# Optimization experiments

Hardware: AMD Instinct MI355X
Metric: run time of the kernel (lower is better)

## Reference

```python
import jax, jax.numpy as jnp
import numpy as np

N_NODES = 50000
N_EDGES = 1000000
HIDDEN = 64
NUM_GRAPHS = 512
EPS = 1e-5


def _instance_norm(x, seg, num_graphs):
    # per-graph, per-channel normalization (PyG InstanceNorm, affine=False)
    ones = jnp.ones((x.shape[0], 1), x.dtype)
    cnt = jnp.clip(jax.ops.segment_sum(ones, seg, num_segments=num_graphs), 1.0)
    mean = jax.ops.segment_sum(x, seg, num_segments=num_graphs) / cnt
    xc = x - mean[seg]
    var = jax.ops.segment_sum(xc * xc, seg, num_segments=num_graphs) / cnt
    return xc * jax.lax.rsqrt(var + EPS)[seg]


def setup_inputs() -> dict:
    key = jax.random.key(0)
    ks = jax.random.split(key, 10)
    emb = jax.random.normal(ks[0], (N_NODES, HIDDEN), jnp.float32)
    edge_index = jax.random.randint(ks[1], (2, N_EDGES), 0, N_NODES, jnp.int64 if jax.config.read('jax_enable_x64') else jnp.int32)
    batch = jnp.sort(jax.random.randint(ks[2], (N_NODES,), 0, NUM_GRAPHS))
    h = HIDDEN
    # channels = [2h, 4h, h, 1]
    W1 = jax.random.normal(ks[3], (2 * h, 4 * h), jnp.float32) * 0.05
    b1 = jnp.zeros((4 * h,), jnp.float32)
    W2 = jax.random.normal(ks[4], (4 * h, h), jnp.float32) * 0.05
    b2 = jnp.zeros((h,), jnp.float32)
    W3 = jax.random.normal(ks[5], (h, 1), jnp.float32) * 0.05
    b3 = jnp.zeros((1,), jnp.float32)
    return {"emb": emb, "W1": W1, "b1": b1, "W2": W2, "b2": b2,
            "W3": W3, "b3": b3, "edge_index": edge_index, "batch": batch}


def reference(emb, W1, b1, W2, b2, W3, b3, edge_index, batch):
    col, row = edge_index[0], edge_index[1]
    f12 = jnp.concatenate([emb[col], emb[row]], axis=-1)  # [E, 2h]
    seg = batch[col]  # per-edge graph id
    x = f12 @ W1 + b1                                      # [E, 4h]
    x = jax.nn.relu(_instance_norm(x, seg, NUM_GRAPHS))
    x = x @ W2 + b2                                        # [E, h]
    x = jax.nn.relu(_instance_norm(x, seg, NUM_GRAPHS))
    return x @ W3 + b3                                     # [E, 1]
```

## Files before the change

kernel.cpp:

```cpp
#include <hip/hip_runtime.h>
#include <hip/hip_bf16.h>

#define EDGES 1000000
#define NNODES 50000
#define NG 512
#define NTILES 15625
#define NCOLB 50176

typedef __attribute__((ext_vector_type(8))) short bf16x8;
typedef __attribute__((ext_vector_type(4))) float f32x4;

__device__ __forceinline__ unsigned short f2bf(float f){
  unsigned u = __float_as_uint(f);
  u += 0x7fffu + ((u >> 16) & 1u);
  return (unsigned short)(u >> 16);
}
__device__ __forceinline__ float bf2f(unsigned short h){
  return __uint_as_float(((unsigned)h) << 16);
}
__device__ __forceinline__ unsigned pk2bf(float x, float y){
  __hip_bfloat162 h = __float22bfloat162_rn(make_float2(x, y));
  union { __hip_bfloat162 h; unsigned u; } cv; cv.h = h;
  return cv.u;
}
__device__ __forceinline__ void gload_lds16(const void* g, void* l){
  __builtin_amdgcn_global_load_lds(
      (const __attribute__((address_space(1))) unsigned int*)g,
      (__attribute__((address_space(3))) unsigned int*)l, 16, 0, 0);
}
__device__ __forceinline__ int xcd_swizzle(int bid, int nb){
  int nb8 = nb & ~7;
  if (bid >= nb8) return bid;
  int per = nb8 >> 3;
  return (bid & 7) * per + (bid >> 3);
}

__global__ void prep_all(const float* __restrict__ emb, const float* __restrict__ W1,
                         const float* __restrict__ W2,
                         unsigned short* __restrict__ emb_bf,
                         unsigned short* __restrict__ w1tn, unsigned short* __restrict__ w2t){
  int i = blockIdx.x * 256 + threadIdx.x;
  if (i < NNODES * 64){
    emb_bf[i] = f2bf(emb[i]);
  } else {
    int j = i - NNODES * 64;
    if (j < 32768){
      int jj = j >> 6, k = j & 63;
      float v = (jj < 256) ? W1[k * 256 + jj] : W1[(k + 64) * 256 + (jj - 256)];
      w1tn[j] = f2bf(v);
    } else {
      int jj = j - 32768;
      if (jj < 16384){
        int n = jj >> 8, p = jj & 255;
        int korig = (p & ~127) | ((p & 7) << 4) | ((p >> 3) & 15);
        w2t[jj] = f2bf(W2[korig * 64 + n]);
      }
    }
  }
}

__global__ void hists(const int* __restrict__ ei, const int* __restrict__ batch,
                      unsigned* __restrict__ hist, unsigned* __restrict__ chist){
  __shared__ unsigned h[NG];
  int t = threadIdx.x;
  h[t] = 0; h[t + 256] = 0;
  __syncthreads();
  for (int i = 0; i < 4; i++){
    int e = blockIdx.x * 1024 + i * 256 + t;
    if (e < EDGES){
      int cn = ei[e];
      atomicAdd(&chist[cn], 1u);
      atomicAdd(&h[batch[cn]], 1u);
    }
  }
  __syncthreads();
  atomicAdd(&hist[t], h[t]);
  atomicAdd(&hist[t + 256], h[t + 256]);
}

__global__ void col_scan1(const unsigned* __restrict__ chist, unsigned* __restrict__ cpre,
                          unsigned* __restrict__ bsum){
  __shared__ unsigned s[256];
  int t = threadIdx.x;
  int i = blockIdx.x * 256 + t;
  unsigned v = (i < NNODES) ? chist[i] : 0u;
  s[t] = v;
  __syncthreads();
  for (int o = 1; o < 256; o <<= 1){
    unsigned u = (t >= o) ? s[t - o] : 0u;
    __syncthreads();
    s[t] += u;
    __syncthreads();
  }
  cpre[i] = s[t] - v;
  if (t == 255) bsum[blockIdx.x] = s[255];
}

__global__ void col_scan2(unsigned* __restrict__ bsum){
  __shared__ unsigned s[256];
  int t = threadIdx.x;
  unsigned v = (t < 196) ? bsum[t] : 0u;
  s[t] = v;
  __syncthreads();
  for (int o = 1; o < 256; o <<= 1){
    unsigned u = (t >= o) ? s[t - o] : 0u;
    __syncthreads();
    s[t] += u;
    __syncthreads();
  }
  if (t < 196) bsum[t] = s[t] - v;
}

__global__ void col_scan3(unsigned* __restrict__ cpre, const unsigned* __restrict__ bsum){
  int i = blockIdx.x * 256 + threadIdx.x;
  cpre[i] += bsum[blockIdx.x];
}

__global__ void col_scatter(const int* __restrict__ ei, const int* __restrict__ batch,
                            unsigned* __restrict__ cpre, int4* __restrict__ emeta){
  for (int i = 0; i < 4; i++){
    int e = blockIdx.x * 1024 + i * 256 + threadIdx.x;
    if (e < EDGES){
      int cn = ei[e];
      int pos = (int)atomicAdd(&cpre[cn], 1u);
      emeta[pos] = make_int4(cn, ei[EDGES + e], batch[cn], e);
    }
  }
}

__global__ __launch_bounds__(256) void node_gemm(
    const unsigned short* __restrict__ emb_bf, const unsigned short* __restrict__ w1tn,
    unsigned short* __restrict__ P)
{
  __shared__ unsigned short As[64 * 72];
  int t = threadIdx.x;
  int n0 = blockIdx.x * 64;
  {
    int nl = t >> 2, part = t & 3;
    int node = n0 + nl; if (node >= NNODES) node = 0;
    const int4* src = (const int4*)(emb_bf + node * 64 + part * 16);
    int4* dst = (int4*)(As + nl * 72 + part * 16);
    dst[0] = src[0]; dst[1] = src[1];
  }
  __syncthreads();
  int w = t >> 6, lane = t & 63, q = lane >> 4, c = lane & 15;
  f32x4 acc[4][8];
  for (int a = 0; a < 4; a++) for (int b = 0; b < 8; b++) for (int r = 0; r < 4; r++) acc[a][b][r] = 0.f;
  for (int k0 = 0; k0 < 64; k0 += 32){
    bf16x8 af[4];
    for (int tt = 0; tt < 4; tt++) af[tt] = *(const bf16x8*)(As + (tt * 16 + c) * 72 + k0 + q * 8);
    for (int n4 = 0; n4 < 8; n4++){
      bf16x8 bw = *(const bf16x8*)(w1tn + (w * 128 + n4 * 16 + c) * 64 + k0 + q * 8);
      for (int tt = 0; tt < 4; tt++)
        acc[tt][n4] = __builtin_amdgcn_mfma_f32_16x16x32_bf16(af[tt], bw, acc[tt][n4], 0, 0, 0);
    }
  }
  for (int tt = 0; tt < 4; tt++){
    for (int r = 0; r < 4; r++){
      int node = n0 + tt * 16 + q * 4 + r;
      if (node < NNODES){
        uint4 pk;
        pk.x = pk2bf(acc[tt][0][r], acc[tt][1][r]);
        pk.y = pk2bf(acc[tt][2][r], acc[tt][3][r]);
        pk.z = pk2bf(acc[tt][4][r], acc[tt][5][r]);
        pk.w = pk2bf(acc[tt][6][r], acc[tt][7][r]);
        *(uint4*)(P + (size_t)node * 512 + w * 128 + c * 8) = pk;
      }
    }
  }
}

__global__ __launch_bounds__(256, 5) void k1_gather(
    const unsigned short* __restrict__ P, const int4* __restrict__ emeta,
    float* __restrict__ sum1, float* __restrict__ sqs1)
{
  __shared__ float ls[1024];
  int t = threadIdx.x;
  int bid = xcd_swizzle(blockIdx.x, gridDim.x);
  int tile0 = bid * 8;
  for (int i = t; i < 1024; i += 256) ls[i] = 0.f;
  int s0 = emeta[tile0 * 64].z;
  int elast = tile0 * 64 + 511; if (elast >= EDGES) elast = EDGES - 1;
  int s1 = emeta[elast].z;
  __syncthreads();

  int w = t >> 6, lane = t & 63, c4 = lane * 4;

  float sm0 = 0.f, sm1 = 0.f, sm2 = 0.f, sm3 = 0.f;
  float q0 = 0.f, q1 = 0.f, q2 = 0.f, q3 = 0.f;
  int curs = -1;

  auto FLUSH = [&](int s){
    if (s == s0 || s == s1){
      float* base = ls + ((s == s0) ? 0 : 512) + c4;
      atomicAdd(base + 0, sm0); atomicAdd(base + 1, sm1);
      atomicAdd(base + 2, sm2); atomicAdd(base + 3, sm3);
      atomicAdd(base + 256, q0); atomicAdd(base + 257, q1);
      atomicAdd(base + 258, q2); atomicAdd(base + 259, q3);
    } else {
      float* sp = sum1 + s * 256 + c4;
      float* qp = sqs1 + s * 256 + c4;
      atomicAdd(sp + 0, sm0); atomicAdd(sp + 1, sm1); atomicAdd(sp + 2, sm2); atomicAdd(sp + 3, sm3);
      atomicAdd(qp + 0, q0);  atomicAdd(qp + 1, q1);  atomicAdd(qp + 2, q2);  atomicAdd(qp + 3, q3);
    }
    sm0 = sm1 = sm2 = sm3 = 0.f; q0 = q1 = q2 = q3 = 0.f;
  };

  for (int ti = 0; ti < 2; ti++){
    int tile = tile0 + w * 2 + ti;
    if (tile >= NTILES) continue;
    int4 me = emeta[tile * 64 + lane];
    int sseg = __builtin_amdgcn_readlane(me.z, 0);
    bool uni = (__ballot(me.z == sseg) == ~0ull);
    if (uni){
      if (sseg != curs){
        if (curs >= 0) FLUSH(curs);
        curs = sseg;
      }
      ushort4 rv[3][4], cv[3][4];
      #pragma unroll
      for (int g = 0; g < 2; g++){
        #pragma unroll
        for (int j = 0; j < 4; j++){
          int e = g * 4 + j;
          int re = __builtin_amdgcn_readlane(me.y, e);
          int ce = __builtin_amdgcn_readlane(me.x, e);
          rv[g][j] = *(const ushort4*)(P + (size_t)re * 512 + 256 + c4);
          cv[g][j] = *(const ushort4*)(P + (size_t)ce * 512 + c4);
        }
      }
      #pragma unroll
      for (int g = 0; g < 16; g++){
        if (g < 14){
          int bn = (g + 2) % 3;
          #pragma unroll
          for (int j = 0; j < 4; j++){
            int e = (g + 2) * 4 + j;
            int re = __builtin_amdgcn_readlane(me.y, e);
            int ce = __builtin_amdgcn_readlane(me.x, e);
            rv[bn][j] = *(const ushort4*)(P + (size_t)re * 512 + 256 + c4);
            cv[bn][j] = *(const ushort4*)(P + (size_t)ce * 512 + c4);
          }
        }
        int b = g % 3;
        #pragma unroll
        for (int j = 0; j < 4; j++){
          float x0 = bf2f(cv[b][j].x) + bf2f(rv[b][j].x);
          float x1 = bf2f(cv[b][j].y) + bf2f(rv[b][j].y);
          float x2v = bf2f(cv[b][j].z) + bf2f(rv[b][j].z);
          float x3 = bf2f(cv[b][j].w) + bf2f(rv[b][j].w);
          sm0 += x0; q0 += x0 * x0;
          sm1 += x1; q1 += x1 * x1;
          sm2 += x2v; q2 += x2v * x2v;
          sm3 += x3; q3 += x3 * x3;
        }
      }
    } else {
      int cprev = -1;
      ushort4 a = make_ushort4(0, 0, 0, 0);
      for (int e = 0; e < 64; e++){
        int ce = __builtin_amdgcn_readlane(me.x, e);
        int re = __builtin_amdgcn_readlane(me.y, e);
        int s = __builtin_amdgcn_readlane(me.z, e);
        if (s != curs){
          if (curs >= 0) FLUSH(curs);
          curs = s;
        }
        if (ce != cprev){ a = *(const ushort4*)(P + (size_t)ce * 512 + c4); cprev = ce; }
        ushort4 b = *(const ushort4*)(P + (size_t)re * 512 + 256 + c4);
        float x0 = bf2f(a.x) + bf2f(b.x);
        float x1 = bf2f(a.y) + bf2f(b.y);
        float x2v = bf2f(a.z) + bf2f(b.z);
        float x3 = bf2f(a.w) + bf2f(b.w);
        sm0 += x0; q0 += x0 * x0;
        sm1 += x1; q1 += x1 * x1;
        sm2 += x2v; q2 += x2v * x2v;
        sm3 += x3; q3 += x3 * x3;
      }
    }
  }
  if (curs >= 0) FLUSH(curs);

  __syncthreads();
  atomicAdd(&sum1[s0 * 256 + t], ls[t]);
  atomicAdd(&sqs1[s0 * 256 + t], ls[256 + t]);
  if (s1 != s0){
    atomicAdd(&sum1[s1 * 256 + t], ls[512 + t]);
    atomicAdd(&sqs1[s1 * 256 + t], ls[768 + t]);
  }
}

__global__ void finalize1(const float* __restrict__ sum1, const float* __restrict__ sqs1,
                          const unsigned* __restrict__ hist, float* __restrict__ r1,
                          float* __restrict__ mr1){
  int i = blockIdx.x * 256 + threadIdx.x;
  int g = i >> 8;
  float cnt = fmaxf((float)hist[g], 1.f);
  float m = sum1[i] / cnt;
  float v = sqs1[i] / cnt - m * m;
  v = fmaxf(v, 0.f);
  float r = rsqrtf(v + 1e-5f);
  r1[i] = r;
  mr1[i] = m * r;
}

__global__ void finalize2(const float* __restrict__ sum2, const float* __restrict__ sqs2,
                          const unsigned* __restrict__ hist, float* __restrict__ r2,
                          float* __restrict__ mr2){
  int i = blockIdx.x * 256 + threadIdx.x;
  int g = i >> 6;
  float cnt = fmaxf((float)hist[g], 1.f);
  float m = sum2[i] / cnt;
  float v = sqs2[i] / cnt - m * m;
  v = fmaxf(v, 0.f);
  float r = rsqrtf(v + 1e-5f);
  r2[i] = r;
  mr2[i] = m * r;
}

__global__ __launch_bounds__(256, 4) void k2_fused(
    const unsigned short* __restrict__ P, const unsigned short* __restrict__ w2t,
    const int4* __restrict__ emeta,
    const float* __restrict__ r1, const float* __restrict__ mr1,
    float* __restrict__ sum2, float* __restrict__ sqs2,
    unsigned short* __restrict__ x2t)
{
  __shared__ unsigned short Y[64 * 256];
  __shared__ int segl[64];
  __shared__ short rsegA[64];
  __shared__ unsigned char rloA[65];
  __shared__ int nrunS;
  int t = threadIdx.x;
  int bid = xcd_swizzle(blockIdx.x, gridDim.x);
  int p0 = bid * 64;
  int w = t >> 6, lane = t & 63, q = lane >> 4, c = lane & 15;
  int c4 = lane * 4;
  int elb0 = w * 16;
  int4 me = emeta[p0 + elb0 + (lane & 15)];

  #pragma unroll
  for (int pp = 0; pp < 8; pp++){
    int r0 = __builtin_amdgcn_readlane(me.y, 2 * pp);
    int r1n = __builtin_amdgcn_readlane(me.y, 2 * pp + 1);
    int node = (lane < 32) ? r0 : r1n;
    const unsigned short* g = P + (size_t)node * 512 + 256 + (lane & 31) * 8;
    gload_lds16(g, &Y[(elb0 + 2 * pp) * 256]);
  }

  int cprev = __builtin_amdgcn_readlane(me.x, 0);
  ushort4 a = *(const ushort4*)(P + (size_t)cprev * 512 + c4);
  int s0g = __builtin_amdgcn_readlane(me.z, 0);
  float4 r4  = *(const float4*)(r1  + s0g * 256 + c4);
  float4 mr4 = *(const float4*)(mr1 + s0g * 256 + c4);

  if (t < 64) segl[t] = emeta[p0 + t].z;
  if (w == 0){
    int sN = segl[lane];
    int nxt = (lane < 63) ? segl[lane + 1] : sN;
    unsigned long long mask = __ballot(sN != nxt);
    if (lane == 0){
      if (mask == 0ull){
        nrunS = 1; rloA[0] = 0; rloA[1] = 64; rsegA[0] = (short)sN;
      } else {
        int n = 0, cur = segl[0];
        rsegA[0] = (short)cur; rloA[0] = 0;
        for (int i = 1; i < 64; i++)
          if (segl[i] != cur){ cur = segl[i]; n++; rsegA[n] = (short)cur; rloA[n] = (unsigned char)i; }
        rloA[n + 1] = 64; nrunS = n + 1;
      }
    }
  }
  __syncthreads();
  int nrun = nrunS;
  bool uni = (nrun == 1);

  ushort4 bb[16];
  #pragma unroll
  for (int e = 0; e < 16; e++)
    bb[e] = *(const ushort4*)(Y + (elb0 + e) * 256 + c4);

  #pragma unroll
  for (int e = 0; e < 16; e++){
    int ce = __builtin_amdgcn_readlane(me.x, e);
    if (ce != cprev){ a = *(const ushort4*)(P + (size_t)ce * 512 + c4); cprev = ce; }
    float4 rr4 = r4, mm4 = mr4;
    if (!uni){
      int s = __builtin_amdgcn_readlane(me.z, e);
      rr4 = *(const float4*)(r1  + s * 256 + c4);
      mm4 = *(const float4*)(mr1 + s * 256 + c4);
    }
    float y0 = fmaxf(0.f, (bf2f(a.x) + bf2f(bb[e].x)) * rr4.x - mm4.x);
    float y1 = fmaxf(0.f, (bf2f(a.y) + bf2f(bb[e].y)) * rr4.y - mm4.y);
    float y2 = fmaxf(0.f, (bf2f(a.z) + bf2f(bb[e].z)) * rr4.z - mm4.z);
    float y3 = fmaxf(0.f, (bf2f(a.w) + bf2f(bb[e].w)) * rr4.w - mm4.w);
    uint2 pk;
    pk.x = pk2bf(y0, y1);
    pk.y = pk2bf(y2, y3);
    int row = elb0 + e;
    *(uint2*)((char*)Y + row * 512 + ((lane * 8) ^ ((row & 7) << 4))) = pk;
  }
  __syncthreads();

  f32x4 acc2[4];
  for (int tt = 0; tt < 4; tt++) for (int r = 0; r < 4; r++) acc2[tt][r] = 0.f;
  int ch2 = w * 16 + c;
  int swzr = (c & 7) << 4;
  for (int kc = 0; kc < 8; kc++){
    bf16x8 bfr = *(const bf16x8*)(w2t + ch2 * 256 + kc * 32 + q * 8);
    int kb = (kc * 64 + q * 16) ^ swzr;
    for (int tt = 0; tt < 4; tt++){
      bf16x8 afr = *(const bf16x8*)((const char*)Y + (tt * 16 + c) * 512 + kb);
      acc2[tt] = __builtin_amdgcn_mfma_f32_16x16x32_bf16(afr, bfr, acc2[tt], 0, 0, 0);
    }
  }

  if (uni){
    int s = segl[0];
    float sm = 0.f, sq = 0.f;
    for (int tt = 0; tt < 4; tt++)
      for (int r = 0; r < 4; r++){
        float v = acc2[tt][r];
        sm += v; sq += v * v;
      }
    sm += __shfl_xor(sm, 16); sq += __shfl_xor(sq, 16);
    sm += __shfl_xor(sm, 32); sq += __shfl_xor(sq, 32);
    if (q == 0){
      atomicAdd(&sum2[s * 64 + ch2], sm);
      atomicAdd(&sqs2[s * 64 + ch2], sq);
    }
  } else {
    for (int rr = 0; rr < nrun; rr++){
      int s = rsegA[rr], lo = rloA[rr], hi = rloA[rr + 1];
      float sm = 0.f, sq = 0.f;
      for (int tt = 0; tt < 4; tt++){
        int elb = tt * 16 + q * 4;
        for (int r = 0; r < 4; r++){
          int el = elb + r;
          if (el >= lo && el < hi){
            float v = acc2[tt][r];
            sm += v; sq += v * v;
          }
        }
      }
      sm += __shfl_xor(sm, 16); sq += __shfl_xor(sq, 16);
      sm += __shfl_xor(sm, 32); sq += __shfl_xor(sq, 32);
      if (q == 0){
        atomicAdd(&sum2[s * 64 + ch2], sm);
        atomicAdd(&sqs2[s * 64 + ch2], sq);
      }
    }
  }
  for (int tt = 0; tt < 4; tt++){
    uint2 pk;
    pk.x = pk2bf(acc2[tt][0], acc2[tt][1]);
    pk.y = pk2bf(acc2[tt][2], acc2[tt][3]);
    *(uint2*)(x2t + (size_t)ch2 * EDGES + p0 + tt * 16 + q * 4) = pk;
  }
}

__global__ __launch_bounds__(256) void k3_out(
    const unsigned short* __restrict__ x2t, const int4* __restrict__ emeta,
    const float* __restrict__ r2, const float* __restrict__ mr2,
    const float* __restrict__ W3, const float* __restrict__ b3, float* __restrict__ out)
{
  int pp4 = (blockIdx.x * 256 + threadIdx.x) * 4;
  if (pp4 >= EDGES) return;
  int4 m0 = emeta[pp4 + 0];
  int4 m1 = emeta[pp4 + 1];
  int4 m2 = emeta[pp4 + 2];
  int4 m3 = emeta[pp4 + 3];
  float a0 = 0.f, a1 = 0.f, a2 = 0.f, a3 = 0.f;
  if (m0.z == m3.z && m0.z == m1.z && m0.z == m2.z){
    const float* rp = r2  + m0.z * 64;
    const float* mp = mr2 + m0.z * 64;
    #pragma unroll 8
    for (int ch = 0; ch < 64; ch++){
      ushort4 v = *(const ushort4*)(x2t + (size_t)ch * EDGES + pp4);
      float rr = rp[ch], mm = mp[ch], wv = W3[ch];
      a0 += fmaxf(0.f, bf2f(v.x) * rr - mm) * wv;
      a1 += fmaxf(0.f, bf2f(v.y) * rr - mm) * wv;
      a2 += fmaxf(0.f, bf2f(v.z) * rr - mm) * wv;
      a3 += fmaxf(0.f, bf2f(v.w) * rr - mm) * wv;
    }
  } else {
    #pragma unroll 8
    for (int ch = 0; ch < 64; ch++){
      ushort4 v = *(const ushort4*)(x2t + (size_t)ch * EDGES + pp4);
      float wv = W3[ch];
      a0 += fmaxf(0.f, bf2f(v.x) * r2[m0.z * 64 + ch] - mr2[m0.z * 64 + ch]) * wv;
      a1 += fmaxf(0.f, bf2f(v.y) * r2[m1.z * 64 + ch] - mr2[m1.z * 64 + ch]) * wv;
      a2 += fmaxf(0.f, bf2f(v.z) * r2[m2.z * 64 + ch] - mr2[m2.z * 64 + ch]) * wv;
      a3 += fmaxf(0.f, bf2f(v.w) * r2[m3.z * 64 + ch] - mr2[m3.z * 64 + ch]) * wv;
    }
  }
  float bv = b3[0];
  out[m0.w] = a0 + bv;
  out[m1.w] = a1 + bv;
  out[m2.w] = a2 + bv;
  out[m3.w] = a3 + bv;
}

extern "C" void kernel_launch(void* const* d_in, const int* in_sizes, int n_in,
                              void* d_out, int out_size, void* d_ws, size_t ws_size,
                              hipStream_t stream)
{
  (void)in_sizes; (void)n_in; (void)out_size;
  const float* emb = (const float*)d_in[0];
  const float* W1  = (const float*)d_in[1];
  const float* W2  = (const float*)d_in[3];
  const float* W3  = (const float*)d_in[5];
  const float* b3  = (const float*)d_in[6];
  const int* ei    = (const int*)d_in[7];
  const int* batch = (const int*)d_in[8];
  float* out = (float*)d_out;

  char* p = (char*)d_ws;
  size_t off = 0;
  auto take = [&](size_t n) -> char* {
    char* r = p + off;
    off += (n + 255) & ~(size_t)255;
    return r;
  };

  unsigned short* emb_bf = (unsigned short*)take((size_t)NNODES * 64 * 2);
  unsigned short* w1tn   = (unsigned short*)take(32768 * 2);
  unsigned short* w2t    = (unsigned short*)take(16384 * 2);
  int4* emeta = (int4*)take((size_t)EDGES * 16);
  unsigned short* P   = (unsigned short*)take((size_t)NNODES * 512 * 2);
  unsigned short* x2t = (unsigned short*)take((size_t)EDGES * 64 * 2);
  float* r1  = (float*)take(512 * 256 * 4);
  float* mr1 = (float*)take(512 * 256 * 4);
  float* r2  = (float*)take(512 * 64 * 4);
  float* mr2 = (float*)take(512 * 64 * 4);
  unsigned* cpre = (unsigned*)take(NCOLB * 4);
  unsigned* bsum = (unsigned*)take(256 * 4);
  char* zbase = p + off;
  unsigned* hist  = (unsigned*)take(NG * 4);
  unsigned* chist = (unsigned*)take(NCOLB * 4);
  float* sum1 = (float*)take(512 * 256 * 4);
  float* sqs1 = (float*)take(512 * 256 * 4);
  float* sum2 = (float*)take(512 * 64 * 4);
  float* sqs2 = (float*)take(512 * 64 * 4);
  size_t zsize = (size_t)((p + off) - zbase);

  if (ws_size < off) return;

  hipMemsetAsync(zbase, 0, zsize, stream);
  prep_all<<<12692, 256, 0, stream>>>(emb, W1, W2, emb_bf, w1tn, w2t);
  hists<<<977, 256, 0, stream>>>(ei, batch, hist, chist);
  col_scan1<<<196, 256, 0, stream>>>(chist, cpre, bsum);
  col_scan2<<<1, 256, 0, stream>>>(bsum);
  col_scan3<<<196, 256, 0, stream>>>(cpre, bsum);
  col_scatter<<<977, 256, 0, stream>>>(ei, batch, cpre, emeta);
  node_gemm<<<(NNODES + 63) / 64, 256, 0, stream>>>(emb_bf, w1tn, P);
  k1_gather<<<(NTILES + 7) / 8, 256, 0, stream>>>(P, emeta, sum1, sqs1);
  finalize1<<<512, 256, 0, stream>>>(sum1, sqs1, hist, r1, mr1);
  k2_fused<<<NTILES, 256, 0, stream>>>(P, w2t, emeta, r1, mr1, sum2, sqs2, x2t);
  finalize2<<<128, 256, 0, stream>>>(sum2, sqs2, hist, r2, mr2);
  k3_out<<<977, 256, 0, stream>>>(x2t, emeta, r2, mr2, W3, b3, out);
}
```

Measured before the change: 495.5 us.

## Merge preprocessing kernels into fewer launches and use nontemporal x2t traffic

Fuses the histogram and bf16 conversion kernels into one launch by splitting blocks by role. It also merges the column scatter with the node GEMM, folding the block-offset scan add into the scatter so the col_scan3 launch goes away. Separately, the x2t intermediate is written and read with nontemporal hints to reduce cache pollution. This cuts three kernel launches and their serialization gaps, at the cost of heterogeneous blocks inside one grid.

```diff
diff --git a/kernel.cpp b/kernel.cpp
--- a/kernel.cpp
+++ b/kernel.cpp
@@ -6,6 +6,8 @@
 #define NG 512
 #define NTILES 15625
 #define NCOLB 50176
+#define HBLK 977
+#define GBLK 782
 
 typedef __attribute__((ext_vector_type(8))) short bf16x8;
 typedef __attribute__((ext_vector_type(4))) float f32x4;
@@ -35,47 +37,48 @@
   return (bid & 7) * per + (bid >> 3);
 }
 
-__global__ void prep_all(const float* __restrict__ emb, const float* __restrict__ W1,
-                         const float* __restrict__ W2,
-                         unsigned short* __restrict__ emb_bf,
-                         unsigned short* __restrict__ w1tn, unsigned short* __restrict__ w2t){
-  int i = blockIdx.x * 256 + threadIdx.x;
-  if (i < NNODES * 64){
-    emb_bf[i] = f2bf(emb[i]);
-  } else {
-    int j = i - NNODES * 64;
-    if (j < 32768){
-      int jj = j >> 6, k = j & 63;
-      float v = (jj < 256) ? W1[k * 256 + jj] : W1[(k + 64) * 256 + (jj - 256)];
-      w1tn[j] = f2bf(v);
-    } else {
-      int jj = j - 32768;
-      if (jj < 16384){
-        int n = jj >> 8, p = jj & 255;
-        int korig = (p & ~127) | ((p & 7) << 4) | ((p >> 3) & 15);
-        w2t[jj] = f2bf(W2[korig * 64 + n]);
-      }
-    }
-  }
-}
-
-__global__ void hists(const int* __restrict__ ei, const int* __restrict__ batch,
-                      unsigned* __restrict__ hist, unsigned* __restrict__ chist){
+__global__ void prep_hists(const float* __restrict__ emb, const float* __restrict__ W1,
+                           const float* __restrict__ W2,
+                           const int* __restrict__ ei, const int* __restrict__ batch,
+                           unsigned short* __restrict__ emb_bf,
+                           unsigned short* __restrict__ w1tn, unsigned short* __restrict__ w2t,
+                           unsigned* __restrict__ hist, unsigned* __restrict__ chist){
   __shared__ unsigned h[NG];
   int t = threadIdx.x;
-  h[t] = 0; h[t + 256] = 0;
-  __syncthreads();
-  for (int i = 0; i < 4; i++){
-    int e = blockIdx.x * 1024 + i * 256 + t;
-    if (e < EDGES){
-      int cn = ei[e];
-      atomicAdd(&chist[cn], 1u);
-      atomicAdd(&h[batch[cn]], 1u);
-    }
-  }
-  __syncthreads();
-  atomicAdd(&hist[t], h[t]);
-  atomicAdd(&hist[t + 256], h[t + 256]);
+  if (blockIdx.x < HBLK){
+    h[t] = 0; h[t + 256] = 0;
+    __syncthreads();
+    for (int i = 0; i < 4; i++){
+      int e = blockIdx.x * 1024 + i * 256 + t;
+      if (e < EDGES){
+        int cn = ei[e];
+        atomicAdd(&chist[cn], 1u);
+        atomicAdd(&h[batch[cn]], 1u);
+      }
+    }
+    __syncthreads();
+    atomicAdd(&hist[t], h[t]);
+    atomicAdd(&hist[t + 256], h[t + 256]);
+  } else {
+    int i = (blockIdx.x - HBLK) * 256 + t;
+    if (i < NNODES * 64){
+      emb_bf[i] = f2bf(emb[i]);
+    } else {
+      int j = i - NNODES * 64;
+      if (j < 32768){
+        int jj = j >> 6, k = j & 63;
+        float v = (jj < 256) ? W1[k * 256 + jj] : W1[(k + 64) * 256 + (jj - 256)];
+        w1tn[j] = f2bf(v);
+      } else {
+        int jj = j - 32768;
+        if (jj < 16384){
+          int n = jj >> 8, p = jj & 255;
+          int korig = (p & ~127) | ((p & 7) << 4) | ((p >> 3) & 15);
+          w2t[jj] = f2bf(W2[korig * 64 + n]);
+        }
+      }
+    }
+  }
 }
 
 __global__ void col_scan1(const unsigned* __restrict__ chist, unsigned* __restrict__ cpre,
@@ -111,30 +114,27 @@
   if (t < 196) bsum[t] = s[t] - v;
 }
 
-__global__ void col_scan3(unsigned* __restrict__ cpre, const unsigned* __restrict__ bsum){
-  int i = blockIdx.x * 256 + threadIdx.x;
-  cpre[i] += bsum[blockIdx.x];
-}
-
-__global__ void col_scatter(const int* __restrict__ ei, const int* __restrict__ batch,
-                            unsigned* __restrict__ cpre, int4* __restrict__ emeta){
-  for (int i = 0; i < 4; i++){
-    int e = blockIdx.x * 1024 + i * 256 + threadIdx.x;
-    if (e < EDGES){
-      int cn = ei[e];
-      int pos = (int)atomicAdd(&cpre[cn], 1u);
-      emeta[pos] = make_int4(cn, ei[EDGES + e], batch[cn], e);
-    }
-  }
-}
-
-__global__ __launch_bounds__(256) void node_gemm(
+__global__ __launch_bounds__(256) void scat_gemm(
+    const int* __restrict__ ei, const int* __restrict__ batch,
+    unsigned* __restrict__ cpre, const unsigned* __restrict__ bsum,
+    int4* __restrict__ emeta,
     const unsigned short* __restrict__ emb_bf, const unsigned short* __restrict__ w1tn,
     unsigned short* __restrict__ P)
 {
   __shared__ unsigned short As[64 * 72];
   int t = threadIdx.x;
-  int n0 = blockIdx.x * 64;
+  if (blockIdx.x < HBLK){
+    for (int i = 0; i < 4; i++){
+      int e = blockIdx.x * 1024 + i * 256 + t;
+      if (e < EDGES){
+        int cn = ei[e];
+        int pos = (int)atomicAdd(&cpre[cn], 1u) + (int)bsum[cn >> 8];
+        emeta[pos] = make_int4(cn, ei[EDGES + e], batch[cn], e);
+      }
+    }
+    return;
+  }
+  int n0 = (blockIdx.x - HBLK) * 64;
   {
     int nl = t >> 2, part = t & 3;
     int node = n0 + nl; if (node >= NNODES) node = 0;
@@ -454,7 +454,9 @@
     uint2 pk;
     pk.x = pk2bf(acc2[tt][0], acc2[tt][1]);
     pk.y = pk2bf(acc2[tt][2], acc2[tt][3]);
-    *(uint2*)(x2t + (size_t)ch2 * EDGES + p0 + tt * 16 + q * 4) = pk;
+    unsigned long long v = (unsigned long long)pk.x | ((unsigned long long)pk.y << 32);
+    __builtin_nontemporal_store(v,
+        (unsigned long long*)(x2t + (size_t)ch2 * EDGES + p0 + tt * 16 + q * 4));
   }
 }
 
@@ -470,12 +472,15 @@
   int4 m2 = emeta[pp4 + 2];
   int4 m3 = emeta[pp4 + 3];
   float a0 = 0.f, a1 = 0.f, a2 = 0.f, a3 = 0.f;
+  union { unsigned long long u; ushort4 s; } cv;
   if (m0.z == m3.z && m0.z == m1.z && m0.z == m2.z){
     const float* rp = r2  + m0.z * 64;
     const float* mp = mr2 + m0.z * 64;
     #pragma unroll 8
     for (int ch = 0; ch < 64; ch++){
-      ushort4 v = *(const ushort4*)(x2t + (size_t)ch * EDGES + pp4);
+      cv.u = __builtin_nontemporal_load(
+          (const unsigned long long*)(x2t + (size_t)ch * EDGES + pp4));
+      ushort4 v = cv.s;
       float rr = rp[ch], mm = mp[ch], wv = W3[ch];
       a0 += fmaxf(0.f, bf2f(v.x) * rr - mm) * wv;
       a1 += fmaxf(0.f, bf2f(v.y) * rr - mm) * wv;
@@ -485,7 +490,9 @@
   } else {
     #pragma unroll 8
     for (int ch = 0; ch < 64; ch++){
-      ushort4 v = *(const ushort4*)(x2t + (size_t)ch * EDGES + pp4);
+      cv.u = __builtin_nontemporal_load(
+          (const unsigned long long*)(x2t + (size_t)ch * EDGES + pp4));
+      ushort4 v = cv.s;
       float wv = W3[ch];
       a0 += fmaxf(0.f, bf2f(v.x) * r2[m0.z * 64 + ch] - mr2[m0.z * 64 + ch]) * wv;
       a1 += fmaxf(0.f, bf2f(v.y) * r2[m1.z * 64 + ch] - mr2[m1.z * 64 + ch]) * wv;
@@ -546,13 +553,12 @@
   if (ws_size < off) return;
 
   hipMemsetAsync(zbase, 0, zsize, stream);
-  prep_all<<<12692, 256, 0, stream>>>(emb, W1, W2, emb_bf, w1tn, w2t);
-  hists<<<977, 256, 0, stream>>>(ei, batch, hist, chist);
+  prep_hists<<<HBLK + 12692, 256, 0, stream>>>(emb, W1, W2, ei, batch,
+                                               emb_bf, w1tn, w2t, hist, chist);
   col_scan1<<<196, 256, 0, stream>>>(chist, cpre, bsum);
   col_scan2<<<1, 256, 0, stream>>>(bsum);
-  col_scan3<<<196, 256, 0, stream>>>(cpre, bsum);
-  col_scatter<<<977, 256, 0, stream>>>(ei, batch, cpre, emeta);
-  node_gemm<<<(NNODES + 63) / 64, 256, 0, stream>>>(emb_bf, w1tn, P);
+  scat_gemm<<<HBLK + GBLK, 256, 0, stream>>>(ei, batch, cpre, bsum, emeta,
+                                             emb_bf, w1tn, P);
   k1_gather<<<(NTILES + 7) / 8, 256, 0, stream>>>(P, emeta, sum1, sqs1);
   finalize1<<<512, 256, 0, stream>>>(sum1, sqs1, hist, r1, mr1);
   k2_fused<<<NTILES, 256, 0, stream>>>(P, w2t, emeta, r1, mr1, sum2, sqs2, x2t);
```

Result: no change. 495.1 us (-0.1%).
